# Performance work log

Hardware: AMD Instinct MI355X
Metric: run time of the kernel (lower is better)

Reference implementation:

```python
import jax, jax.numpy as jnp
import numpy as np
from jax import lax

B, C, H, W = 16, 128, 128, 128
COUT, KH, KW, K, RED, TEMP = 128, 3, 3, 4, 4, 30.0
ATTN_CH = max(C // RED, 1)

def setup_inputs() -> dict:
    key = jax.random.key(0)
    ks = jax.random.split(key, 7)
    fan_out = COUT * KH * KW
    std = np.sqrt(2.0 / fan_out)  # kaiming_normal fan_out, relu
    return {
        "x": jax.random.normal(ks[0], (B, C, H, W), dtype=jnp.float32),
        "weight": jax.random.normal(ks[1], (K, COUT, C, KH, KW), dtype=jnp.float32) * std,
        "bias": jnp.zeros((K, COUT), dtype=jnp.float32),
        "aw1": jax.random.normal(ks[2], (ATTN_CH, C), dtype=jnp.float32) * (1.0 / np.sqrt(C)),
        "ab1": jnp.zeros((ATTN_CH,), dtype=jnp.float32),
        "aw2": jax.random.normal(ks[3], (K, ATTN_CH), dtype=jnp.float32) * (1.0 / np.sqrt(ATTN_CH)),
        "ab2": jnp.zeros((K,), dtype=jnp.float32),
    }

def reference(x, weight, bias, aw1, ab1, aw2, ab2):
    # Attention branch: global avg pool -> 1x1 conv -> relu -> 1x1 conv
    pooled = jnp.mean(x, axis=(2, 3))                       # (B, C)
    h = jax.nn.relu(pooled @ aw1.T + ab1)                   # (B, attn_ch)
    scores = h @ aw2.T + ab2                                # (B, K)
    attn = jax.nn.softmax(scores / TEMP, axis=1)            # (B, K)

    # Per-sample aggregated kernel and bias
    agg_w = jnp.einsum('bk,koipq->boipq', attn, weight)     # (B, Cout, Cin, kH, kW)
    agg_b = attn @ bias                                     # (B, Cout)

    # Per-sample conv2d (stride 1, padding 1, dilation 1, groups 1)
    def conv_one(xi, wi):
        return lax.conv_general_dilated(
            xi[None], wi,
            window_strides=(1, 1),
            padding=((1, 1), (1, 1)),
            dimension_numbers=('NCHW', 'OIHW', 'NCHW'),
        )[0]

    out = jax.vmap(conv_one)(x, agg_w)                      # (B, Cout, H, W)
    return out + agg_b[:, :, None, None]
```

## Files before the change

### kernel.cpp

```cpp
#include <hip/hip_runtime.h>

typedef float f32x4 __attribute__((ext_vector_type(4)));
typedef short bf16x8 __attribute__((ext_vector_type(8)));

__device__ __forceinline__ unsigned short f2bf(float f) {
  unsigned u = __builtin_bit_cast(unsigned, f);
  u = (u + 0x7FFFu + ((u >> 16) & 1u)) >> 16;
  return (unsigned short)u;
}

__device__ __forceinline__ void async16(const unsigned short* g, unsigned short* l) {
  __builtin_amdgcn_global_load_lds(
      (__attribute__((address_space(1))) void*)g,
      (__attribute__((address_space(3))) void*)l, 16, 0, 0);
}

#define XT_ROW 16640

__global__ __launch_bounds__(256) void k_transpose(const float* __restrict__ x,
                                                   unsigned short* __restrict__ xt,
                                                   float* __restrict__ rowsum) {
  __shared__ unsigned short tile[128][128];
  __shared__ float psum[128][8];
  const int y = blockIdx.x, b = blockIdx.y;
  const int t = threadIdx.x;
  const int colb = (t & 7) * 16;
  const int cp = t >> 3;
  const int swz = (t & 7) << 3;
  for (int ci = 0; ci < 4; ++ci) {
    const int c = ci * 32 + cp;
    const int c2 = c ^ swz;
    const float* src = x + (((size_t)(b * 128 + c) * 128 + y) * 128 + colb);
    float s = 0.f;
#pragma unroll
    for (int j = 0; j < 16; j += 4) {
      float4 v = *(const float4*)(src + j);
      s += v.x + v.y + v.z + v.w;
      tile[colb + j + 0][c2] = f2bf(v.x);
      tile[colb + j + 1][c2] = f2bf(v.y);
      tile[colb + j + 2][c2] = f2bf(v.z);
      tile[colb + j + 3][c2] = f2bf(v.w);
    }
    psum[c][t & 7] = s;
  }
  __syncthreads();
#pragma unroll
  for (int it = 0; it < 8; ++it) {
    const int slot = t + it * 256;
    const int col = slot >> 4;
    const int cg = (slot & 15) * 8;
    const int c2 = cg ^ (((col >> 4) & 7) << 3);
    uint4 vv = *(const uint4*)&tile[col][c2];
    *(uint4*)(xt + (((size_t)b * 130 + y + 1) * 130 + col + 1) * 128 + cg) = vv;
  }
  if (t < 128) {
    float r = 0.f;
#pragma unroll
    for (int j = 0; j < 8; ++j) r += psum[t][j];
    rowsum[((size_t)b * 128 + t) * 128 + y] = r;
  }
}

__global__ __launch_bounds__(256) void k_border(unsigned short* __restrict__ xt) {
  const int b = blockIdx.y;
  const int idx = blockIdx.x * 256 + threadIdx.x;
  if (idx >= 8256) return;
  int row, col, ck;
  if (idx < 4160) {
    row = (idx < 2080) ? 0 : 129;
    const int s = idx % 2080;
    col = s >> 4;
    ck = s & 15;
  } else {
    const int s = idx - 4160;
    row = (s >> 5) + 1;
    col = (s & 16) ? 129 : 0;
    ck = s & 15;
  }
  uint4 z = {0, 0, 0, 0};
  *(uint4*)(xt + ((size_t)b * 130 + row) * 130 * 128 + (size_t)col * 128 + ck * 8) = z;
}

__global__ __launch_bounds__(128) void k_attn(const float* __restrict__ rowsum,
                                              const float* __restrict__ aw1,
                                              const float* __restrict__ ab1,
                                              const float* __restrict__ aw2,
                                              const float* __restrict__ ab2,
                                              const float* __restrict__ bias,
                                              float* __restrict__ attn,
                                              float* __restrict__ aggb) {
  __shared__ float pooled[128];
  __shared__ float h[32];
  __shared__ float at[4];
  const int b = blockIdx.x, t = threadIdx.x;
  const float* rs = rowsum + (size_t)(b * 128 + t) * 128;
  float s = 0.f;
  for (int yy = 0; yy < 128; ++yy) s += rs[yy];
  pooled[t] = s * (1.f / 16384.f);
  __syncthreads();
  if (t < 32) {
    float hv = ab1[t];
    for (int c = 0; c < 128; ++c) hv += pooled[c] * aw1[t * 128 + c];
    h[t] = fmaxf(hv, 0.f);
  }
  __syncthreads();
  if (t < 4) {
    float sc = ab2[t];
    for (int a = 0; a < 32; ++a) sc += h[a] * aw2[t * 32 + a];
    at[t] = sc * (1.f / 30.f);
  }
  __syncthreads();
  if (t == 0) {
    float m = fmaxf(fmaxf(at[0], at[1]), fmaxf(at[2], at[3]));
    float e0 = __expf(at[0] - m), e1 = __expf(at[1] - m);
    float e2 = __expf(at[2] - m), e3 = __expf(at[3] - m);
    float inv = 1.f / (e0 + e1 + e2 + e3);
    at[0] = e0 * inv; at[1] = e1 * inv; at[2] = e2 * inv; at[3] = e3 * inv;
  }
  __syncthreads();
  if (t < 4) attn[b * 4 + t] = at[t];
  float ab = 0.f;
  for (int k = 0; k < 4; ++k) ab += at[k] * bias[k * 128 + t];
  aggb[b * 128 + t] = ab;
}

__global__ __launch_bounds__(256) void k_aggw(const float* __restrict__ weight,
                                              const float* __restrict__ attn,
                                              unsigned short* __restrict__ aggw) {
  const int fid = blockIdx.x * 256 + threadIdx.x;
  const int kk = fid & 31;
  const int o = (fid >> 5) & 127;
  const int rest = fid >> 12;
  const int s = rest % 36;
  const int b = rest / 36;
  const int c = ((s & 3) << 5) + kk;
  const int pq = s >> 2;
  const size_t src = (size_t)o * 1152 + (size_t)c * 9 + pq;
  float v = attn[b * 4 + 0] * weight[src]
          + attn[b * 4 + 1] * weight[src + 147456]
          + attn[b * 4 + 2] * weight[src + 2 * 147456]
          + attn[b * 4 + 3] * weight[src + 3 * 147456];
  aggw[fid] = f2bf(v);
}

__global__ __launch_bounds__(512, 2) void k_conv(const unsigned short* __restrict__ xt,
                                                 const unsigned short* __restrict__ aggw,
                                                 const float* __restrict__ aggb,
                                                 float* __restrict__ out) {
  __shared__ unsigned short lds[78848];
  const int id = blockIdx.x;
  const int swz = (id & 7) * 128 + (id >> 3);
  const int b = swz >> 6;
  const int y0 = (swz & 63) * 2;
  const int t = threadIdx.x;
  const int lane = t & 63, w = t >> 6;
  const int mw = w >> 2, nw = w & 3;
  const int l15 = lane & 15, lk = lane >> 4;

  {
    const unsigned short* xb = xt + (size_t)(b * 130 + y0) * XT_ROW;
#pragma unroll
    for (int i = 0; i < 16; ++i) {
      const int idx = i * 512 + t;
      const int row = idx / 2080, rem = idx % 2080;
      const int col = rem >> 4, k8 = rem & 15;
      async16(xb + (row * 130 + col) * 128 + ((k8 ^ (col & 15)) * 8),
              &lds[0] + i * 4096 + w * 512);
    }
    if (w < 2) {
      const int idx = 8192 + t;
      const int row = idx / 2080, rem = idx % 2080;
      const int col = rem >> 4, k8 = rem & 15;
      async16(xb + (row * 130 + col) * 128 + ((k8 ^ (col & 15)) * 8),
              &lds[0] + 65536 + w * 512);
    }
  }
  const int an = t >> 2, ak8 = t & 3;
  const unsigned short* aS = aggw + (size_t)b * 147456 + an * 32
                           + ((ak8 ^ ((an >> 1) & 3)) * 8);
  unsigned short* aldsw = &lds[66560] + w * 512;

#define STAGE_A(buf, s) async16(aS + (s) * 4096, aldsw + (buf) * 4096)

  STAGE_A(0, 0);
  STAGE_A(1, 1);

  const int rbase = (nw >> 1) * 16640;
  const int px0 = (nw & 1) * 64 + l15;
  f32x4 acc[4][4] = {};

#pragma unroll
  for (int s = 0; s < 36; ++s) {
    const int tap = s >> 2, cc = s & 3;
    const int p = tap / 3, q = tap - 3 * p;
    if (s < 35) { asm volatile("s_waitcnt vmcnt(1)" ::: "memory"); }
    else        { asm volatile("s_waitcnt vmcnt(0)" ::: "memory"); }
    __builtin_amdgcn_sched_barrier(0);
    __builtin_amdgcn_s_barrier();
    __builtin_amdgcn_sched_barrier(0);

    const unsigned short* A0 = &lds[66560 + (s % 3) * 4096];
    bf16x8 af[4], bfr[4];
#pragma unroll
    for (int mi = 0; mi < 4; ++mi) {
      const int row = mw * 64 + mi * 16 + l15;
      af[mi] = *(const bf16x8*)(A0 + row * 32 + ((lk ^ ((row >> 1) & 3)) * 8));
    }
#pragma unroll
    for (int ni = 0; ni < 4; ++ni) {
      const int col = px0 + ni * 16 + q;
      bfr[ni] = *(const bf16x8*)(&lds[0] + rbase + p * 16640 + col * 128
                                 + (((cc * 4 + lk) ^ (col & 15)) * 8));
    }
    if (s + 2 < 36) STAGE_A((s + 2) % 3, s + 2);
    __builtin_amdgcn_sched_barrier(0);
    asm volatile("s_waitcnt lgkmcnt(0)" ::: "memory");
    __builtin_amdgcn_sched_barrier(0);
    __builtin_amdgcn_s_setprio(1);
#pragma unroll
    for (int mi = 0; mi < 4; ++mi)
#pragma unroll
      for (int ni = 0; ni < 4; ++ni)
        acc[mi][ni] = __builtin_amdgcn_mfma_f32_16x16x32_bf16(af[mi], bfr[ni], acc[mi][ni], 0, 0, 0);
    __builtin_amdgcn_s_setprio(0);
    __builtin_amdgcn_sched_barrier(0);
  }
#undef STAGE_A

  const int y = y0 + (nw >> 1);
  const int colb = (nw & 1) * 64 + l15;
#pragma unroll
  for (int mi = 0; mi < 4; ++mi) {
    const int o = mw * 64 + mi * 16 + lk * 4;
#pragma unroll
    for (int rr = 0; rr < 4; ++rr) {
      const float bsv = aggb[b * 128 + o + rr];
      float* orow = out + ((size_t)(b * 128 + o + rr) * 128 + y) * 128 + colb;
      orow[0]  = acc[mi][0][rr] + bsv;
      orow[16] = acc[mi][1][rr] + bsv;
      orow[32] = acc[mi][2][rr] + bsv;
      orow[48] = acc[mi][3][rr] + bsv;
    }
  }
}

extern "C" void kernel_launch(void* const* d_in, const int* in_sizes, int n_in,
                              void* d_out, int out_size, void* d_ws, size_t ws_size,
                              hipStream_t stream) {
  const float* x      = (const float*)d_in[0];
  const float* weight = (const float*)d_in[1];
  const float* bias   = (const float*)d_in[2];
  const float* aw1    = (const float*)d_in[3];
  const float* ab1    = (const float*)d_in[4];
  const float* aw2    = (const float*)d_in[5];
  const float* ab2    = (const float*)d_in[6];
  float* out = (float*)d_out;

  char* ws = (char*)d_ws;
  unsigned short* xt   = (unsigned short*)ws;
  unsigned short* aggw = (unsigned short*)(ws + 69222400);
  float* rowsum        = (float*)(ws + 69222400 + 4718592);
  float* attn          = (float*)(ws + 69222400 + 4718592 + 1048576);
  float* aggb          = (float*)(ws + 69222400 + 4718592 + 1048576 + 256);

  hipLaunchKernelGGL(k_border, dim3(33, 16), dim3(256), 0, stream, xt);
  hipLaunchKernelGGL(k_transpose, dim3(128, 16), dim3(256), 0, stream, x, xt, rowsum);
  hipLaunchKernelGGL(k_attn, dim3(16), dim3(128), 0, stream,
                     rowsum, aw1, ab1, aw2, ab2, bias, attn, aggb);
  hipLaunchKernelGGL(k_aggw, dim3(9216), dim3(256), 0, stream, weight, attn, aggw);
  hipLaunchKernelGGL(k_conv, dim3(1024), dim3(512), 0, stream, xt, aggw, aggb, out);
}
```

Measured before the change: 154.4 us.

## Process two K-stages per barrier with 4-buffer weight ring and unpadded LDS tile

Restructures the conv main loop to handle two reduction stages per barrier, using a four-slot weight ring so two stages are prefetched per iteration and barriers are halved. The input tile in LDS now drops the padded border columns, which are handled by clamping the address and zeroing the edge fragments. This simplifies the load index math and removes the extra tail load. Launch bounds drop from two blocks per CU to one because LDS grows, trading occupancy for fewer syncs. The loop also waits on all outstanding loads each iteration, which may expose load latency.

```diff
diff --git a/kernel.cpp b/kernel.cpp
--- a/kernel.cpp
+++ b/kernel.cpp
@@ -143,11 +143,11 @@
   aggw[fid] = f2bf(v);
 }
 
-__global__ __launch_bounds__(512, 2) void k_conv(const unsigned short* __restrict__ xt,
+__global__ __launch_bounds__(512, 1) void k_conv(const unsigned short* __restrict__ xt,
                                                  const unsigned short* __restrict__ aggw,
                                                  const float* __restrict__ aggb,
                                                  float* __restrict__ out) {
-  __shared__ unsigned short lds[78848];
+  __shared__ unsigned short lds[81920];
   const int id = blockIdx.x;
   const int swz = (id & 7) * 128 + (id >> 3);
   const int b = swz >> 6;
@@ -162,72 +162,69 @@
 #pragma unroll
     for (int i = 0; i < 16; ++i) {
       const int idx = i * 512 + t;
-      const int row = idx / 2080, rem = idx % 2080;
-      const int col = rem >> 4, k8 = rem & 15;
-      async16(xb + (row * 130 + col) * 128 + ((k8 ^ (col & 15)) * 8),
+      const int row = idx >> 11, col = (idx >> 4) & 127, k8 = idx & 15;
+      async16(xb + (row * 130 + col + 1) * 128 + ((k8 ^ (col & 15)) * 8),
               &lds[0] + i * 4096 + w * 512);
-    }
-    if (w < 2) {
-      const int idx = 8192 + t;
-      const int row = idx / 2080, rem = idx % 2080;
-      const int col = rem >> 4, k8 = rem & 15;
-      async16(xb + (row * 130 + col) * 128 + ((k8 ^ (col & 15)) * 8),
-              &lds[0] + 65536 + w * 512);
     }
   }
   const int an = t >> 2, ak8 = t & 3;
   const unsigned short* aS = aggw + (size_t)b * 147456 + an * 32
                            + ((ak8 ^ ((an >> 1) & 3)) * 8);
-  unsigned short* aldsw = &lds[66560] + w * 512;
+  unsigned short* aldsw = &lds[65536] + w * 512;
 
 #define STAGE_A(buf, s) async16(aS + (s) * 4096, aldsw + (buf) * 4096)
 
   STAGE_A(0, 0);
   STAGE_A(1, 1);
 
-  const int rbase = (nw >> 1) * 16640;
+  const int r_ = nw >> 1;
   const int px0 = (nw & 1) * 64 + l15;
   f32x4 acc[4][4] = {};
 
 #pragma unroll
-  for (int s = 0; s < 36; ++s) {
-    const int tap = s >> 2, cc = s & 3;
-    const int p = tap / 3, q = tap - 3 * p;
-    if (s < 35) { asm volatile("s_waitcnt vmcnt(1)" ::: "memory"); }
-    else        { asm volatile("s_waitcnt vmcnt(0)" ::: "memory"); }
+  for (int g = 0; g < 18; ++g) {
+    asm volatile("s_waitcnt vmcnt(0)" ::: "memory");
     __builtin_amdgcn_sched_barrier(0);
     __builtin_amdgcn_s_barrier();
     __builtin_amdgcn_sched_barrier(0);
-
-    const unsigned short* A0 = &lds[66560 + (s % 3) * 4096];
-    bf16x8 af[4], bfr[4];
-#pragma unroll
-    for (int mi = 0; mi < 4; ++mi) {
-      const int row = mw * 64 + mi * 16 + l15;
-      af[mi] = *(const bf16x8*)(A0 + row * 32 + ((lk ^ ((row >> 1) & 3)) * 8));
-    }
-#pragma unroll
-    for (int ni = 0; ni < 4; ++ni) {
-      const int col = px0 + ni * 16 + q;
-      bfr[ni] = *(const bf16x8*)(&lds[0] + rbase + p * 16640 + col * 128
-                                 + (((cc * 4 + lk) ^ (col & 15)) * 8));
-    }
-    if (s + 2 < 36) STAGE_A((s + 2) % 3, s + 2);
+    if (g + 1 < 18) { STAGE_A((2 * g + 2) & 3, 2 * g + 2);
+                      STAGE_A((2 * g + 3) & 3, 2 * g + 3); }
     __builtin_amdgcn_sched_barrier(0);
-    asm volatile("s_waitcnt lgkmcnt(0)" ::: "memory");
-    __builtin_amdgcn_sched_barrier(0);
-    __builtin_amdgcn_s_setprio(1);
-#pragma unroll
-    for (int mi = 0; mi < 4; ++mi)
-#pragma unroll
-      for (int ni = 0; ni < 4; ++ni)
-        acc[mi][ni] = __builtin_amdgcn_mfma_f32_16x16x32_bf16(af[mi], bfr[ni], acc[mi][ni], 0, 0, 0);
-    __builtin_amdgcn_s_setprio(0);
-    __builtin_amdgcn_sched_barrier(0);
+#pragma unroll
+    for (int ss = 0; ss < 2; ++ss) {
+      const int s = 2 * g + ss;
+      const int tap = s >> 2, cc = s & 3;
+      const int p = tap / 3, q = tap - 3 * p;
+      const unsigned short* A0 = &lds[65536 + (s & 3) * 4096];
+      bf16x8 af[4], bfr[4];
+#pragma unroll
+      for (int mi = 0; mi < 4; ++mi) {
+        const int row = mw * 64 + mi * 16 + l15;
+        af[mi] = *(const bf16x8*)(A0 + row * 32 + ((lk ^ ((row >> 1) & 3)) * 8));
+      }
+#pragma unroll
+      for (int ni = 0; ni < 4; ++ni) {
+        const int icol = px0 + ni * 16 + q - 1;
+        int ccl = icol;
+        if (q == 0 && ni == 0) ccl = (icol < 0) ? 0 : icol;
+        if (q == 2 && ni == 3) ccl = (icol > 127) ? 127 : icol;
+        bfr[ni] = *(const bf16x8*)(&lds[0] + ((r_ + p) * 128 + ccl) * 128
+                                   + (((cc * 4 + lk) ^ (ccl & 15)) * 8));
+        if (q == 0 && ni == 0) { if (icol < 0)   bfr[ni] = (bf16x8)0; }
+        if (q == 2 && ni == 3) { if (icol > 127) bfr[ni] = (bf16x8)0; }
+      }
+      __builtin_amdgcn_s_setprio(1);
+#pragma unroll
+      for (int mi = 0; mi < 4; ++mi)
+#pragma unroll
+        for (int ni = 0; ni < 4; ++ni)
+          acc[mi][ni] = __builtin_amdgcn_mfma_f32_16x16x32_bf16(af[mi], bfr[ni], acc[mi][ni], 0, 0, 0);
+      __builtin_amdgcn_s_setprio(0);
+    }
   }
 #undef STAGE_A
 
-  const int y = y0 + (nw >> 1);
+  const int y = y0 + r_;
   const int colb = (nw & 1) * 64 + l15;
 #pragma unroll
   for (int mi = 0; mi < 4; ++mi) {
```

Result: no change. 155.8 us (+0.9%).

## Restructure conv tiling to stream halo-shifted input tiles per stage

Applied to the files above, without the earlier changes.

The conv kernel now gives each block four output rows, 512 blocks in total, instead of two rows across 1024 blocks. Each wave computes all 128 output channels for 64 pixels. The kernel no longer preloads the whole halo input window into LDS. Each of the 36 reduction stages streams both the weight slice and a tap-shifted input slice into a triple-buffered LDS ring, with the loads split across two barrier-separated MFMA half-phases. This reuses each weight fragment across more pixels, but it re-reads input data from global/L2 once per tap and adds more barriers per stage.

```diff
diff --git a/kernel.cpp b/kernel.cpp
--- a/kernel.cpp
+++ b/kernel.cpp
@@ -147,91 +147,113 @@
                                                  const unsigned short* __restrict__ aggw,
                                                  const float* __restrict__ aggb,
                                                  float* __restrict__ out) {
-  __shared__ unsigned short lds[78848];
+  __shared__ unsigned short lds[61440];
   const int id = blockIdx.x;
-  const int swz = (id & 7) * 128 + (id >> 3);
-  const int b = swz >> 6;
-  const int y0 = (swz & 63) * 2;
+  const int swz = (id & 7) * 64 + (id >> 3);
+  const int b = swz >> 5;
+  const int Y = (swz & 31) * 4;
   const int t = threadIdx.x;
-  const int lane = t & 63, w = t >> 6;
-  const int mw = w >> 2, nw = w & 3;
+  const int lane = t & 63, nw = t >> 6, w = t >> 6;
   const int l15 = lane & 15, lk = lane >> 4;
-
+  const int xc = (lk ^ ((l15 >> 1) & 3)) * 8;
+  const int aBase = l15 * 32 + xc;
+  const int nrow = (nw >> 1) * 128 + (nw & 1) * 64 + l15;
+  const int bBase = 4096 + nrow * 32 + xc;
+
+  const unsigned short* aS;
   {
-    const unsigned short* xb = xt + (size_t)(b * 130 + y0) * XT_ROW;
-#pragma unroll
-    for (int i = 0; i < 16; ++i) {
-      const int idx = i * 512 + t;
-      const int row = idx / 2080, rem = idx % 2080;
-      const int col = rem >> 4, k8 = rem & 15;
-      async16(xb + (row * 130 + col) * 128 + ((k8 ^ (col & 15)) * 8),
-              &lds[0] + i * 4096 + w * 512);
-    }
-    if (w < 2) {
-      const int idx = 8192 + t;
-      const int row = idx / 2080, rem = idx % 2080;
-      const int col = rem >> 4, k8 = rem & 15;
-      async16(xb + (row * 130 + col) * 128 + ((k8 ^ (col & 15)) * 8),
-              &lds[0] + 65536 + w * 512);
-    }
-  }
-  const int an = t >> 2, ak8 = t & 3;
-  const unsigned short* aS = aggw + (size_t)b * 147456 + an * 32
-                           + ((ak8 ^ ((an >> 1) & 3)) * 8);
-  unsigned short* aldsw = &lds[66560] + w * 512;
-
-#define STAGE_A(buf, s) async16(aS + (s) * 4096, aldsw + (buf) * 4096)
-
-  STAGE_A(0, 0);
-  STAGE_A(1, 1);
-
-  const int rbase = (nw >> 1) * 16640;
-  const int px0 = (nw & 1) * 64 + l15;
-  f32x4 acc[4][4] = {};
+    const int o = t >> 2, k8 = t & 3;
+    aS = aggw + (size_t)b * 147456 + o * 32 + ((k8 ^ ((o >> 1) & 3)) * 8);
+  }
+  const unsigned short* bS[4];
+#pragma unroll
+  for (int i = 0; i < 4; ++i) {
+    const int c = i * 512 + t, n = c >> 2, k8 = c & 3;
+    const int r = n >> 7, col = n & 127;
+    bS[i] = xt + ((size_t)(b * 130 + Y + r) * 130 + col) * 128
+          + ((k8 ^ ((n >> 1) & 3)) * 8);
+  }
+
+#define STA(jb, sv) async16(aS + (size_t)(sv) * 4096, &lds[(jb) + w * 512])
+#define STB(jb, bo, i) async16(bS[i] + (bo), &lds[(jb) + 4096 + ((i) * 512 + w * 64) * 8])
+#define BOFF(sv) (((sv) >> 2) / 3 * XT_ROW + (((sv) >> 2) - 3 * (((sv) >> 2) / 3)) * 128 \
+                  + (((sv) & 3) << 5))
+
+  STA(0, 0);
+#pragma unroll
+  for (int i = 0; i < 4; ++i) STB(0, BOFF(0), i);
+  STA(20480, 1);
+#pragma unroll
+  for (int i = 0; i < 4; ++i) STB(20480, BOFF(1), i);
+
+  f32x4 acc[8][4] = {};
 
 #pragma unroll
   for (int s = 0; s < 36; ++s) {
-    const int tap = s >> 2, cc = s & 3;
-    const int p = tap / 3, q = tap - 3 * p;
-    if (s < 35) { asm volatile("s_waitcnt vmcnt(1)" ::: "memory"); }
+    const int jb = (s % 3) * 20480;
+    const int j2 = ((s + 2) % 3) * 20480;
+    const int s2 = s + 2;
+    const bool st = (s2 < 36);
+    const int bo2 = st ? BOFF(s2) : 0;
+
+    if (s < 35) { asm volatile("s_waitcnt vmcnt(5)" ::: "memory"); }
     else        { asm volatile("s_waitcnt vmcnt(0)" ::: "memory"); }
     __builtin_amdgcn_sched_barrier(0);
     __builtin_amdgcn_s_barrier();
     __builtin_amdgcn_sched_barrier(0);
-
-    const unsigned short* A0 = &lds[66560 + (s % 3) * 4096];
-    bf16x8 af[4], bfr[4];
-#pragma unroll
-    for (int mi = 0; mi < 4; ++mi) {
-      const int row = mw * 64 + mi * 16 + l15;
-      af[mi] = *(const bf16x8*)(A0 + row * 32 + ((lk ^ ((row >> 1) & 3)) * 8));
-    }
+    if (st) { STA(j2, s2); STB(j2, bo2, 0); STB(j2, bo2, 1); }
+
+    bf16x8 a0, a1, a2, a3, b0, b1, b2, b3;
+    b0 = *(const bf16x8*)(&lds[jb + bBase + 0 * 512]);
+    b1 = *(const bf16x8*)(&lds[jb + bBase + 1 * 512]);
+    b2 = *(const bf16x8*)(&lds[jb + bBase + 2 * 512]);
+    b3 = *(const bf16x8*)(&lds[jb + bBase + 3 * 512]);
+    a0 = *(const bf16x8*)(&lds[jb + aBase + 0 * 512]);
+    a1 = *(const bf16x8*)(&lds[jb + aBase + 1 * 512]);
+    a2 = *(const bf16x8*)(&lds[jb + aBase + 2 * 512]);
+    a3 = *(const bf16x8*)(&lds[jb + aBase + 3 * 512]);
+    __builtin_amdgcn_sched_barrier(0);
+    __builtin_amdgcn_s_barrier();
+    __builtin_amdgcn_sched_barrier(0);
+    __builtin_amdgcn_s_setprio(1);
 #pragma unroll
     for (int ni = 0; ni < 4; ++ni) {
-      const int col = px0 + ni * 16 + q;
-      bfr[ni] = *(const bf16x8*)(&lds[0] + rbase + p * 16640 + col * 128
-                                 + (((cc * 4 + lk) ^ (col & 15)) * 8));
-    }
-    if (s + 2 < 36) STAGE_A((s + 2) % 3, s + 2);
-    __builtin_amdgcn_sched_barrier(0);
-    asm volatile("s_waitcnt lgkmcnt(0)" ::: "memory");
+      const bf16x8 bb = (ni == 0) ? b0 : (ni == 1) ? b1 : (ni == 2) ? b2 : b3;
+      acc[0][ni] = __builtin_amdgcn_mfma_f32_16x16x32_bf16(a0, bb, acc[0][ni], 0, 0, 0);
+      acc[1][ni] = __builtin_amdgcn_mfma_f32_16x16x32_bf16(a1, bb, acc[1][ni], 0, 0, 0);
+      acc[2][ni] = __builtin_amdgcn_mfma_f32_16x16x32_bf16(a2, bb, acc[2][ni], 0, 0, 0);
+      acc[3][ni] = __builtin_amdgcn_mfma_f32_16x16x32_bf16(a3, bb, acc[3][ni], 0, 0, 0);
+    }
+    __builtin_amdgcn_s_setprio(0);
+    __builtin_amdgcn_s_barrier();
+    a0 = *(const bf16x8*)(&lds[jb + aBase + 4 * 512]);
+    a1 = *(const bf16x8*)(&lds[jb + aBase + 5 * 512]);
+    a2 = *(const bf16x8*)(&lds[jb + aBase + 6 * 512]);
+    a3 = *(const bf16x8*)(&lds[jb + aBase + 7 * 512]);
+    if (st) { STB(j2, bo2, 2); STB(j2, bo2, 3); }
+    __builtin_amdgcn_sched_barrier(0);
+    __builtin_amdgcn_s_barrier();
     __builtin_amdgcn_sched_barrier(0);
     __builtin_amdgcn_s_setprio(1);
 #pragma unroll
-    for (int mi = 0; mi < 4; ++mi)
-#pragma unroll
-      for (int ni = 0; ni < 4; ++ni)
-        acc[mi][ni] = __builtin_amdgcn_mfma_f32_16x16x32_bf16(af[mi], bfr[ni], acc[mi][ni], 0, 0, 0);
+    for (int ni = 0; ni < 4; ++ni) {
+      const bf16x8 bb = (ni == 0) ? b0 : (ni == 1) ? b1 : (ni == 2) ? b2 : b3;
+      acc[4][ni] = __builtin_amdgcn_mfma_f32_16x16x32_bf16(a0, bb, acc[4][ni], 0, 0, 0);
+      acc[5][ni] = __builtin_amdgcn_mfma_f32_16x16x32_bf16(a1, bb, acc[5][ni], 0, 0, 0);
+      acc[6][ni] = __builtin_amdgcn_mfma_f32_16x16x32_bf16(a2, bb, acc[6][ni], 0, 0, 0);
+      acc[7][ni] = __builtin_amdgcn_mfma_f32_16x16x32_bf16(a3, bb, acc[7][ni], 0, 0, 0);
+    }
     __builtin_amdgcn_s_setprio(0);
-    __builtin_amdgcn_sched_barrier(0);
-  }
-#undef STAGE_A
-
-  const int y = y0 + (nw >> 1);
+  }
+#undef STA
+#undef STB
+#undef BOFF
+
+  const int y = Y + (nw >> 1);
   const int colb = (nw & 1) * 64 + l15;
 #pragma unroll
-  for (int mi = 0; mi < 4; ++mi) {
-    const int o = mw * 64 + mi * 16 + lk * 4;
+  for (int mi = 0; mi < 8; ++mi) {
+    const int o = mi * 16 + lk * 4;
 #pragma unroll
     for (int rr = 0; rr < 4; ++rr) {
       const float bsv = aggb[b * 128 + o + rr];
@@ -268,5 +290,5 @@
   hipLaunchKernelGGL(k_attn, dim3(16), dim3(128), 0, stream,
                      rowsum, aw1, ab1, aw2, ab2, bias, attn, aggb);
   hipLaunchKernelGGL(k_aggw, dim3(9216), dim3(256), 0, stream, weight, attn, aggw);
-  hipLaunchKernelGGL(k_conv, dim3(1024), dim3(512), 0, stream, xt, aggw, aggb, out);
-}
+  hipLaunchKernelGGL(k_conv, dim3(512), dim3(512), 0, stream, xt, aggw, aggb, out);
+}
```

Result: no change. 156.5 us (+1.4%).
